# Kernel tuning notes

Measured on AMD Instinct MI355X. Metric: run time of the kernel, lower is better.

## Reference

```python
import jax, jax.numpy as jnp
import numpy as np

N = 100000
E = 1600000
D_IN = 128
D_H = 128
N_LAYERS = 3


def setup_inputs() -> dict:
    key = jax.random.key(0)
    ks = jax.random.split(key, 4 + 3 * N_LAYERS)
    x = jax.random.normal(ks[0], (N, D_IN), dtype=jnp.float32)
    edge_index = jax.random.randint(ks[1], (2, E), 0, N, dtype=jnp.int64)
    inp = {"x": x, "edge_index": edge_index}
    d_prev = D_IN
    for i in range(N_LAYERS):
        s = 1.0 / np.sqrt(d_prev)
        inp[f"w_rel{i}"] = jax.random.normal(ks[2 + 3 * i], (D_H, d_prev), dtype=jnp.float32) * s
        inp[f"b_rel{i}"] = jnp.zeros((D_H,), dtype=jnp.float32)
        inp[f"w_root{i}"] = jax.random.normal(ks[3 + 3 * i], (D_H, d_prev), dtype=jnp.float32) * s
        d_prev = D_H
    inp["w_out"] = jax.random.normal(ks[-2], (1, D_H), dtype=jnp.float32) / np.sqrt(D_H)
    inp["b_out"] = jnp.zeros((1,), dtype=jnp.float32)
    return inp


def _graph_conv(x, src, dst, w_rel, b_rel, w_root):
    # PyG GraphConv: out_i = W_rel @ sum_{j->i} x_j + b_rel + W_root @ x_i
    msg = x[src]                                        # [E, d] gather
    aggr = jax.ops.segment_sum(msg, dst, num_segments=N)  # [N, d] scatter-add
    return aggr @ w_rel.T + b_rel + x @ w_root.T


def reference(x, edge_index, w_rel0, b_rel0, w_root0, w_rel1, b_rel1, w_root1,
              w_rel2, b_rel2, w_root2, w_out, b_out):
    src, dst = edge_index[0], edge_index[1]
    params = [(w_rel0, b_rel0, w_root0), (w_rel1, b_rel1, w_root1), (w_rel2, b_rel2, w_root2)]
    h = x
    for w_rel, b_rel, w_root in params:
        h = jax.nn.relu(_graph_conv(h, src, dst, w_rel, b_rel, w_root))
    return h @ w_out.T + b_out  # [N, 1]
```

## Files before the change

### kernel.cpp

```cpp
#include <hip/hip_runtime.h>

constexpr int N_NODES = 100000;
constexpr int N_EDGES = 1600000;
constexpr int CAP = 64;
constexpr int NPB = 128;
constexpr int NBIN = (N_NODES + NPB - 1) / NPB;
constexpr int NGRP = 32;
constexpr int SEGCAP = 128;
constexpr int NBLK_A = 1024;
constexpr int EPB = (N_EDGES + NBLK_A - 1) / NBLK_A;
constexpr int CONV_BLKS = (N_NODES * 64) / 256;
constexpr int GCNT_BLKS = (NBIN * NGRP + 255) / 256;

typedef short short8 __attribute__((ext_vector_type(8)));
typedef float f32x4 __attribute__((ext_vector_type(4)));
typedef unsigned int uint4v __attribute__((ext_vector_type(4)));

__device__ __forceinline__ unsigned short f2bf(float f) {
    unsigned int u = __float_as_uint(f);
    unsigned int r = (u + 0x7fff + ((u >> 16) & 1)) >> 16;
    return (unsigned short)r;
}
__device__ __forceinline__ float bflo(unsigned int u) { return __uint_as_float(u << 16); }
__device__ __forceinline__ float bfhi(unsigned int u) { return __uint_as_float(u & 0xffff0000u); }


__global__ __launch_bounds__(256) void prep(const float* __restrict__ x,
                                            unsigned short* __restrict__ A,
                                            const float* __restrict__ wrel0,
                                            const float* __restrict__ wroot0,
                                            const float* __restrict__ wrel1,
                                            const float* __restrict__ wroot1,
                                            const float* __restrict__ wrel2,
                                            const float* __restrict__ wroot2,
                                            unsigned short* __restrict__ pW,
                                            int* __restrict__ gcnt) {
    int b = blockIdx.x;
    if (b < CONV_BLKS) {
        int i = b * 256 + threadIdx.x;
        int node = i >> 6, c2 = (i & 63) * 2;
        float2 v = *(const float2*)&x[(size_t)node * 128 + c2];
        unsigned int out = (unsigned int)f2bf(v.x) | ((unsigned int)f2bf(v.y) << 16);
        *(unsigned int*)&A[(size_t)node * 256 + 128 + c2] = out;
    } else if (b < CONV_BLKS + 384) {
        int bb = b - CONV_BLKS;
        int layer = bb >> 7;
        int t = (bb & 127) * 256 + threadIdx.x;
        const float* wrel  = (layer == 0) ? wrel0  : (layer == 1) ? wrel1  : wrel2;
        const float* wroot = (layer == 0) ? wroot0 : (layer == 1) ? wroot1 : wroot2;
        int j = t & 7, lane = (t >> 3) & 63, ks = (t >> 9) & 7, nt = (t >> 12) & 7;
        int k = ks * 32 + ((lane >> 4) << 3) + j;
        int n = nt * 16 + (lane & 15);
        float v = (k < 128) ? wrel[n * 128 + k] : wroot[n * 128 + (k - 128)];
        pW[(size_t)layer * 32768 + t] = f2bf(v);
    } else {
        int idx = (b - CONV_BLKS - 384) * 256 + threadIdx.x;
        if (idx < NBIN * NGRP) gcnt[idx] = 0;
    }
}

__global__ __launch_bounds__(256) void partition_pairs(const int* __restrict__ src,
                                                       const int* __restrict__ dst,
                                                       int* __restrict__ gcnt,
                                                       int* __restrict__ pairs) {
    __shared__ int hist[NBIN];
    __shared__ int bl[NBIN];
    for (int j = threadIdx.x; j < NBIN; j += 256) hist[j] = 0;
    __syncthreads();
    int base = blockIdx.x * EPB;
    int grp = blockIdx.x >> 5;
    int pv[7], pr[7], pb[7];
    bool val[7];
    #pragma unroll
    for (int k = 0; k < 7; ++k) {
        int off = k * 256 + threadIdx.x;
        int e = base + off;
        val[k] = (off < EPB) && (e < N_EDGES);
        pv[k] = pr[k] = pb[k] = 0;
        if (val[k]) {
            int d = __builtin_nontemporal_load(dst + e);
            int s = __builtin_nontemporal_load(src + e);
            pb[k] = d >> 7;
            pv[k] = ((d & 127) << 17) | s;
            pr[k] = atomicAdd(&hist[pb[k]], 1);
        }
    }
    __syncthreads();
    for (int j = threadIdx.x; j < NBIN; j += 256) {
        int h = hist[j];
        bl[j] = h ? atomicAdd(&gcnt[j * NGRP + grp], h) : 0;
    }
    __syncthreads();
    #pragma unroll
    for (int k = 0; k < 7; ++k)
        if (val[k]) {
            int idx = bl[pb[k]] + pr[k];
            if (idx < SEGCAP)
                pairs[((size_t)pb[k] * NGRP + grp) * SEGCAP + idx] = pv[k];
        }
}

__global__ __launch_bounds__(256) void bucket_build(const int* __restrict__ gcnt,
                                                    const int* __restrict__ pairs,
                                                    int* __restrict__ cnt,
                                                    int* __restrict__ bkt) {
    __shared__ int cnt_l[NPB];
    __shared__ int bkt_l[NPB * CAP];
    int j = blockIdx.x;
    for (int t = threadIdx.x; t < NPB; t += 256) cnt_l[t] = 0;
    __syncthreads();
    int wave = threadIdx.x >> 6, lane = threadIdx.x & 63;
    for (int g = wave; g < NGRP; g += 4) {
        int n = gcnt[j * NGRP + g];
        n = (n > SEGCAP) ? SEGCAP : n;
        const int* seg = pairs + ((size_t)j * NGRP + g) * SEGCAP;
        for (int k = lane; k < n; k += 64) {
            int p = __builtin_nontemporal_load(seg + k);
            int dl = p >> 17;
            int s = p & 0x1FFFF;
            int pos = atomicAdd(&cnt_l[dl], 1);
            if (pos < CAP) bkt_l[(dl << 6) + pos] = s;
        }
    }
    __syncthreads();
    int base_node = j * NPB;
    for (int idx = threadIdx.x; idx < NPB * 16; idx += 256) {
        int node = base_node + (idx >> 4);
        if (node < N_NODES)
            ((uint4*)bkt)[(size_t)node * 16 + (idx & 15)] = ((const uint4*)bkt_l)[idx];
    }
    for (int t = threadIdx.x; t < NPB; t += 256) {
        int node = base_node + t;
        if (node < N_NODES) cnt[node] = cnt_l[t];
    }
}

__global__ __launch_bounds__(256) void gather_bucket(const int* __restrict__ cnt_arr,
                                                     const int* __restrict__ bkt,
                                                     unsigned short* __restrict__ A) {
    int wid = (blockIdx.x * 256 + threadIdx.x) >> 6;
    int lane = threadIdx.x & 63;
    if (wid >= N_NODES) return;
    int cnt = __builtin_nontemporal_load(cnt_arr + wid);
    cnt = (cnt > CAP) ? CAP : cnt;
    int myidx = __builtin_nontemporal_load(bkt + (wid << 6) + lane);
    int g = lane >> 4;
    int ch = lane & 15;
    float acc[8] = {};
    int e = 0;
    for (; e + 16 <= cnt; e += 16) {
        int s0 = __shfl(myidx, e + g);
        int s1 = __shfl(myidx, e + 4 + g);
        int s2 = __shfl(myidx, e + 8 + g);
        int s3 = __shfl(myidx, e + 12 + g);
        uint4 u0 = *(const uint4*)&A[(size_t)s0 * 256 + 128 + ch * 8];
        uint4 u1 = *(const uint4*)&A[(size_t)s1 * 256 + 128 + ch * 8];
        uint4 u2 = *(const uint4*)&A[(size_t)s2 * 256 + 128 + ch * 8];
        uint4 u3 = *(const uint4*)&A[(size_t)s3 * 256 + 128 + ch * 8];
        acc[0] += bflo(u0.x) + bflo(u1.x) + bflo(u2.x) + bflo(u3.x);
        acc[1] += bfhi(u0.x) + bfhi(u1.x) + bfhi(u2.x) + bfhi(u3.x);
        acc[2] += bflo(u0.y) + bflo(u1.y) + bflo(u2.y) + bflo(u3.y);
        acc[3] += bfhi(u0.y) + bfhi(u1.y) + bfhi(u2.y) + bfhi(u3.y);
        acc[4] += bflo(u0.z) + bflo(u1.z) + bflo(u2.z) + bflo(u3.z);
        acc[5] += bfhi(u0.z) + bfhi(u1.z) + bfhi(u2.z) + bfhi(u3.z);
        acc[6] += bflo(u0.w) + bflo(u1.w) + bflo(u2.w) + bflo(u3.w);
        acc[7] += bfhi(u0.w) + bfhi(u1.w) + bfhi(u2.w) + bfhi(u3.w);
    }
    for (; e + 8 <= cnt; e += 8) {
        int s0 = __shfl(myidx, e + g);
        int s1 = __shfl(myidx, e + 4 + g);
        uint4 u0 = *(const uint4*)&A[(size_t)s0 * 256 + 128 + ch * 8];
        uint4 u1 = *(const uint4*)&A[(size_t)s1 * 256 + 128 + ch * 8];
        acc[0] += bflo(u0.x) + bflo(u1.x);
        acc[1] += bfhi(u0.x) + bfhi(u1.x);
        acc[2] += bflo(u0.y) + bflo(u1.y);
        acc[3] += bfhi(u0.y) + bfhi(u1.y);
        acc[4] += bflo(u0.z) + bflo(u1.z);
        acc[5] += bfhi(u0.z) + bfhi(u1.z);
        acc[6] += bflo(u0.w) + bflo(u1.w);
        acc[7] += bfhi(u0.w) + bfhi(u1.w);
    }
    for (; e < cnt; e += 4) {
        int ei = e + g;
        int s0 = __shfl(myidx, ei & 63);
        if (ei < cnt) {
            uint4 u0 = *(const uint4*)&A[(size_t)s0 * 256 + 128 + ch * 8];
            acc[0] += bflo(u0.x); acc[1] += bfhi(u0.x);
            acc[2] += bflo(u0.y); acc[3] += bfhi(u0.y);
            acc[4] += bflo(u0.z); acc[5] += bfhi(u0.z);
            acc[6] += bflo(u0.w); acc[7] += bfhi(u0.w);
        }
    }
    #pragma unroll
    for (int j = 0; j < 8; ++j) {
        acc[j] += __shfl_xor(acc[j], 16);
        acc[j] += __shfl_xor(acc[j], 32);
    }
    if (g == 0) {
        uint4v o;
        o.x = (unsigned int)f2bf(acc[0]) | ((unsigned int)f2bf(acc[1]) << 16);
        o.y = (unsigned int)f2bf(acc[2]) | ((unsigned int)f2bf(acc[3]) << 16);
        o.z = (unsigned int)f2bf(acc[4]) | ((unsigned int)f2bf(acc[5]) << 16);
        o.w = (unsigned int)f2bf(acc[6]) | ((unsigned int)f2bf(acc[7]) << 16);
        __builtin_nontemporal_store(o, (uint4v*)&A[(size_t)wid * 256 + ch * 8]);
    }
}

template <bool LAST>
__global__ __launch_bounds__(256) void mfma_transform(unsigned short* __restrict__ A,
                                                      const unsigned short* __restrict__ packedW,
                                                      const float* __restrict__ brel,
                                                      const float* __restrict__ w_out,
                                                      const float* __restrict__ b_out,
                                                      float* __restrict__ outF) {
    __shared__ unsigned short sW[32768];
    {
        const uint4* g = (const uint4*)packedW;
        uint4* s = (uint4*)sW;
        for (int i = threadIdx.x; i < 4096; i += 256) s[i] = g[i];
    }
    __syncthreads();
    int wave = threadIdx.x >> 6, lane = threadIdx.x & 63;
    int l15 = lane & 15, lhi = lane >> 4;
    int brow = blockIdx.x * 256 + wave * 64;
    float bias[8], wo[8];
    #pragma unroll
    for (int nt = 0; nt < 8; ++nt) {
        bias[nt] = brel[nt * 16 + l15];
        if (LAST) wo[nt] = w_out[nt * 16 + l15];
    }
    float bout = LAST ? b_out[0] : 0.f;

    for (int rtp = 0; rtp < 2; ++rtp) {
        int r0 = brow + rtp * 32;
        short8 a[2][8];
        #pragma unroll
        for (int rt = 0; rt < 2; ++rt) {
            int row = r0 + rt * 16 + l15;
            if (row >= N_NODES) row = N_NODES - 1;
            const unsigned short* ap = &A[(size_t)row * 256 + lhi * 8];
            #pragma unroll
            for (int ks = 0; ks < 8; ++ks) a[rt][ks] = *(const short8*)(ap + ks * 32);
        }
        f32x4 acc[2][8] = {};
        #pragma unroll
        for (int nt = 0; nt < 8; ++nt) {
            #pragma unroll
            for (int ks = 0; ks < 8; ++ks) {
                short8 b = *(const short8*)&sW[(size_t)((nt * 8 + ks) * 64 + lane) * 8];
                acc[0][nt] = __builtin_amdgcn_mfma_f32_16x16x32_bf16(a[0][ks], b, acc[0][nt], 0, 0, 0);
                acc[1][nt] = __builtin_amdgcn_mfma_f32_16x16x32_bf16(a[1][ks], b, acc[1][nt], 0, 0, 0);
            }
        }
        #pragma unroll
        for (int rt = 0; rt < 2; ++rt) {
            if (LAST) {
                #pragma unroll
                for (int rg = 0; rg < 4; ++rg) {
                    float p = 0.f;
                    #pragma unroll
                    for (int nt = 0; nt < 8; ++nt)
                        p += fmaxf(acc[rt][nt][rg] + bias[nt], 0.f) * wo[nt];
                    p += __shfl_xor(p, 1);
                    p += __shfl_xor(p, 2);
                    p += __shfl_xor(p, 4);
                    p += __shfl_xor(p, 8);
                    int row = r0 + rt * 16 + lhi * 4 + rg;
                    if (l15 == 0 && row < N_NODES) outF[row] = p + bout;
                }
            } else {
                #pragma unroll
                for (int nt = 0; nt < 8; ++nt) {
                    #pragma unroll
                    for (int rg = 0; rg < 4; ++rg) {
                        int row = r0 + rt * 16 + lhi * 4 + rg;
                        if (row < N_NODES) {
                            float v = fmaxf(acc[rt][nt][rg] + bias[nt], 0.f);
                            A[(size_t)row * 256 + 128 + nt * 16 + l15] = f2bf(v);
                        }
                    }
                }
            }
        }
    }
}

extern "C" void kernel_launch(void* const* d_in, const int* in_sizes, int n_in,
                              void* d_out, int out_size, void* d_ws, size_t ws_size,
                              hipStream_t stream) {
    const float* x      = (const float*)d_in[0];
    const int*   edge   = (const int*)d_in[1];
    const int*   src    = edge;
    const int*   dst    = edge + N_EDGES;
    const float* w_rel[3]  = {(const float*)d_in[2], (const float*)d_in[5], (const float*)d_in[8]};
    const float* b_rel[3]  = {(const float*)d_in[3], (const float*)d_in[6], (const float*)d_in[9]};
    const float* w_root[3] = {(const float*)d_in[4], (const float*)d_in[7], (const float*)d_in[10]};
    const float* w_out  = (const float*)d_in[11];
    const float* b_out  = (const float*)d_in[12];

    unsigned short* A  = (unsigned short*)d_ws;
    unsigned short* pW = A + (size_t)N_NODES * 256;
    int* cnt   = (int*)(pW + 3 * 32768);
    int* bkt   = cnt + N_NODES;
    int* gcnt  = bkt + (size_t)N_NODES * CAP;
    int* pairs = gcnt + NBIN * NGRP;

    prep<<<CONV_BLKS + 384 + GCNT_BLKS, 256, 0, stream>>>(x, A, w_rel[0], w_root[0],
                                                          w_rel[1], w_root[1],
                                                          w_rel[2], w_root[2], pW, gcnt);

    partition_pairs<<<NBLK_A, 256, 0, stream>>>(src, dst, gcnt, pairs);
    bucket_build<<<NBIN, 256, 0, stream>>>(gcnt, pairs, cnt, bkt);

    const int gblocks = (N_NODES * 64 + 255) / 256;
    const int xblocks = (N_NODES + 255) / 256;

    gather_bucket<<<gblocks, 256, 0, stream>>>(cnt, bkt, A);
    mfma_transform<false><<<xblocks, 256, 0, stream>>>(A, pW + 0 * 32768, b_rel[0],
                                                       nullptr, nullptr, nullptr);
    gather_bucket<<<gblocks, 256, 0, stream>>>(cnt, bkt, A);
    mfma_transform<false><<<xblocks, 256, 0, stream>>>(A, pW + 1 * 32768, b_rel[1],
                                                       nullptr, nullptr, nullptr);
    gather_bucket<<<gblocks, 256, 0, stream>>>(cnt, bkt, A);
    mfma_transform<true><<<xblocks, 256, 0, stream>>>(A, pW + 2 * 32768, b_rel[2],
                                                      w_out, b_out, (float*)d_out);
}
```

Before: 352.7 us.

## Halve MFMA weight smem by staging output halves, add occupancy hint

The transform kernel now keeps only half the packed weights (32 KB instead of 64 KB) in shared memory at a time. For each 32-row tile it loops over two output-column halves, reloading that half of the weights with barriers around it. The LAST-layer dot product is accumulated across halves. Launch bounds request 3 blocks per CU to raise occupancy, and the aggregation store changes from a nontemporal store to a plain one. The cost is re-reading the weights from global/L2 into shared memory four times per block, plus extra barriers.

```diff
diff --git a/kernel.cpp b/kernel.cpp
--- a/kernel.cpp
+++ b/kernel.cpp
@@ -14,7 +14,6 @@
 
 typedef short short8 __attribute__((ext_vector_type(8)));
 typedef float f32x4 __attribute__((ext_vector_type(4)));
-typedef unsigned int uint4v __attribute__((ext_vector_type(4)));
 
 __device__ __forceinline__ unsigned short f2bf(float f) {
     unsigned int u = __float_as_uint(f);
@@ -197,29 +196,23 @@
         acc[j] += __shfl_xor(acc[j], 32);
     }
     if (g == 0) {
-        uint4v o;
+        uint4 o;
         o.x = (unsigned int)f2bf(acc[0]) | ((unsigned int)f2bf(acc[1]) << 16);
         o.y = (unsigned int)f2bf(acc[2]) | ((unsigned int)f2bf(acc[3]) << 16);
         o.z = (unsigned int)f2bf(acc[4]) | ((unsigned int)f2bf(acc[5]) << 16);
         o.w = (unsigned int)f2bf(acc[6]) | ((unsigned int)f2bf(acc[7]) << 16);
-        __builtin_nontemporal_store(o, (uint4v*)&A[(size_t)wid * 256 + ch * 8]);
+        *(uint4*)&A[(size_t)wid * 256 + ch * 8] = o;
     }
 }
 
 template <bool LAST>
-__global__ __launch_bounds__(256) void mfma_transform(unsigned short* __restrict__ A,
-                                                      const unsigned short* __restrict__ packedW,
-                                                      const float* __restrict__ brel,
-                                                      const float* __restrict__ w_out,
-                                                      const float* __restrict__ b_out,
-                                                      float* __restrict__ outF) {
-    __shared__ unsigned short sW[32768];
-    {
-        const uint4* g = (const uint4*)packedW;
-        uint4* s = (uint4*)sW;
-        for (int i = threadIdx.x; i < 4096; i += 256) s[i] = g[i];
-    }
-    __syncthreads();
+__global__ __launch_bounds__(256, 3) void mfma_transform(unsigned short* __restrict__ A,
+                                                         const unsigned short* __restrict__ packedW,
+                                                         const float* __restrict__ brel,
+                                                         const float* __restrict__ w_out,
+                                                         const float* __restrict__ b_out,
+                                                         float* __restrict__ outF) {
+    __shared__ unsigned short sW[16384];
     int wave = threadIdx.x >> 6, lane = threadIdx.x & 63;
     int l15 = lane & 15, lhi = lane >> 4;
     int brow = blockIdx.x * 256 + wave * 64;
@@ -242,43 +235,61 @@
             #pragma unroll
             for (int ks = 0; ks < 8; ++ks) a[rt][ks] = *(const short8*)(ap + ks * 32);
         }
-        f32x4 acc[2][8] = {};
+        float pacc[2][4];
         #pragma unroll
-        for (int nt = 0; nt < 8; ++nt) {
-            #pragma unroll
-            for (int ks = 0; ks < 8; ++ks) {
-                short8 b = *(const short8*)&sW[(size_t)((nt * 8 + ks) * 64 + lane) * 8];
-                acc[0][nt] = __builtin_amdgcn_mfma_f32_16x16x32_bf16(a[0][ks], b, acc[0][nt], 0, 0, 0);
-                acc[1][nt] = __builtin_amdgcn_mfma_f32_16x16x32_bf16(a[1][ks], b, acc[1][nt], 0, 0, 0);
+        for (int rt = 0; rt < 2; ++rt)
+            #pragma unroll
+            for (int rg = 0; rg < 4; ++rg) pacc[rt][rg] = 0.f;
+
+        for (int half = 0; half < 2; ++half) {
+            __syncthreads();
+            {
+                const uint4* gsrc = (const uint4*)(packedW + (size_t)half * 16384);
+                uint4* s = (uint4*)sW;
+                for (int i = threadIdx.x; i < 2048; i += 256) s[i] = gsrc[i];
             }
-        }
-        #pragma unroll
-        for (int rt = 0; rt < 2; ++rt) {
-            if (LAST) {
+            __syncthreads();
+            f32x4 acc[2][4] = {};
+            #pragma unroll
+            for (int ntl = 0; ntl < 4; ++ntl) {
+                #pragma unroll
+                for (int ks = 0; ks < 8; ++ks) {
+                    short8 b = *(const short8*)&sW[(size_t)((ntl * 8 + ks) * 64 + lane) * 8];
+                    acc[0][ntl] = __builtin_amdgcn_mfma_f32_16x16x32_bf16(a[0][ks], b, acc[0][ntl], 0, 0, 0);
+                    acc[1][ntl] = __builtin_amdgcn_mfma_f32_16x16x32_bf16(a[1][ks], b, acc[1][ntl], 0, 0, 0);
+                }
+            }
+            #pragma unroll
+            for (int rt = 0; rt < 2; ++rt) {
+                #pragma unroll
+                for (int ntl = 0; ntl < 4; ++ntl) {
+                    int nt = half * 4 + ntl;
+                    #pragma unroll
+                    for (int rg = 0; rg < 4; ++rg) {
+                        float v = fmaxf(acc[rt][ntl][rg] + bias[nt], 0.f);
+                        if (LAST) {
+                            pacc[rt][rg] += v * wo[nt];
+                        } else {
+                            int row = r0 + rt * 16 + lhi * 4 + rg;
+                            if (row < N_NODES)
+                                A[(size_t)row * 256 + 128 + nt * 16 + l15] = f2bf(v);
+                        }
+                    }
+                }
+            }
+        }
+        if (LAST) {
+            #pragma unroll
+            for (int rt = 0; rt < 2; ++rt) {
                 #pragma unroll
                 for (int rg = 0; rg < 4; ++rg) {
-                    float p = 0.f;
-                    #pragma unroll
-                    for (int nt = 0; nt < 8; ++nt)
-                        p += fmaxf(acc[rt][nt][rg] + bias[nt], 0.f) * wo[nt];
+                    float p = pacc[rt][rg];
                     p += __shfl_xor(p, 1);
                     p += __shfl_xor(p, 2);
                     p += __shfl_xor(p, 4);
                     p += __shfl_xor(p, 8);
                     int row = r0 + rt * 16 + lhi * 4 + rg;
                     if (l15 == 0 && row < N_NODES) outF[row] = p + bout;
-                }
-            } else {
-                #pragma unroll
-                for (int nt = 0; nt < 8; ++nt) {
-                    #pragma unroll
-                    for (int rg = 0; rg < 4; ++rg) {
-                        int row = r0 + rt * 16 + lhi * 4 + rg;
-                        if (row < N_NODES) {
-                            float v = fmaxf(acc[rt][nt][rg] + bias[nt], 0.f);
-                            A[(size_t)row * 256 + 128 + nt * 16 + l15] = f2bf(v);
-                        }
-                    }
                 }
             }
         }
```

Result: faster. 324.8 us (-7.9%).
